# Optimization experiments

Hardware: AMD Instinct MI355X
Metric: run time of the kernel (lower is better)

## Reference

```python
import jax, jax.numpy as jnp
import numpy as np
from functools import partial

# dims matching init_kwargs
H = 512      # hidden_size
F = 2048     # ff_size
NH = 8       # num_heads
NL = 6       # num_layers
V = 1024     # vocab_size
T = 8        # sentence_length
S = 5        # n_sentences_in_paragraph
P = 16       # n_paragraphs_in_article
L = P * S * T          # article_length = 640
N = L + 1              # sequence length used by masks = 641
B = 16                 # batch
HD = H // NH           # head dim
LN_EPS = 1e-5
NEG = -1e9


def _build_mask():
    # pseudo_causal_masks[0] from the torch __init__: causal ~tril plus
    # blocking of within-paragraph sentence-0 key columns.
    a = np.ones((P, S, T, P, S, T), dtype=bool)
    j = np.arange(P)
    a[j, :, :, j, 0, :] = False
    a = a.reshape(L, L)
    causal = ~np.tril(np.ones((N, N), dtype=bool))
    m = causal.copy()
    m[:-1, 1:] = np.logical_and(a, causal[:-1, 1:])
    return m  # True = disallowed


def _build_pe():
    # sinusoidal pe exactly as in __init__ (div_term uses hidden_size in denom)
    pos = np.arange(N, dtype=np.float32)[:, None]
    div = np.exp(np.arange(0, H // 2, dtype=np.float32) * (-np.log(10000.0) / H))
    pe = np.zeros((N, H), dtype=np.float32)
    pe[:, 0::2] = np.sin(pos * div)
    pe[:, 1::2] = np.cos(pos * div)
    return pe


def setup_inputs() -> dict:
    key = jax.random.key(0)
    ks = jax.random.split(key, 12)
    sd = 0.02
    inp = {
        'tokens': jax.random.randint(ks[0], (B, N), 0, V),
        'attn_mask': jnp.asarray(_build_mask()),
        'pe': jnp.asarray(_build_pe()),
        'emb': jax.random.normal(ks[1], (V, H), jnp.float32) * sd,
        'qkv_w': jax.random.normal(ks[2], (NL, 3 * H, H), jnp.float32) * sd,
        'qkv_b': jnp.zeros((NL, 3 * H), jnp.float32),
        'out_w': jax.random.normal(ks[3], (NL, H, H), jnp.float32) * sd,
        'out_b': jnp.zeros((NL, H), jnp.float32),
        'ln1_g': jnp.ones((NL, H), jnp.float32),
        'ln1_b': jnp.zeros((NL, H), jnp.float32),
        'fc1_w': jax.random.normal(ks[4], (NL, F, H), jnp.float32) * sd,
        'fc1_b': jnp.zeros((NL, F), jnp.float32),
        'fc2_w': jax.random.normal(ks[5], (NL, H, F), jnp.float32) * sd,
        'fc2_b': jnp.zeros((NL, H), jnp.float32),
        'ln2_g': jnp.ones((NL, H), jnp.float32),
        'ln2_b': jnp.zeros((NL, H), jnp.float32),
        'lnf_g': jnp.ones((H,), jnp.float32),
        'lnf_b': jnp.zeros((H,), jnp.float32),
        'dep_w': jax.random.normal(ks[6], (V, H), jnp.float32) * sd,
        'dep_b': jnp.zeros((V,), jnp.float32),
    }
    return inp


def _ln(x, g, b):
    m = jnp.mean(x, axis=-1, keepdims=True)
    v = jnp.mean(jnp.square(x - m), axis=-1, keepdims=True)
    return (x - m) * jax.lax.rsqrt(v + LN_EPS) * g + b


def _encoder_layer(x, p, mask):
    qw, qb, ow, ob, g1, b1, w1, bb1, w2, bb2, g2, b2 = p
    Bsz, Nn, _ = x.shape
    qkv = x @ qw.T + qb                                   # [B,N,3H]
    q, k, v = jnp.split(qkv, 3, axis=-1)
    q = q.reshape(Bsz, Nn, NH, HD)
    k = k.reshape(Bsz, Nn, NH, HD)
    v = v.reshape(Bsz, Nn, NH, HD)
    scores = jnp.einsum('bqhd,bkhd->bhqk', q, k) / jnp.sqrt(jnp.asarray(HD, x.dtype))
    scores = jnp.where(mask[None, None], NEG, scores)
    att = jax.nn.softmax(scores, axis=-1)
    o = jnp.einsum('bhqk,bkhd->bqhd', att, v).reshape(Bsz, Nn, H)
    o = o @ ow.T + ob
    x = _ln(x + o, g1, b1)                                # post-LN (torch default)
    f = jax.nn.gelu(x @ w1.T + bb1, approximate=False) @ w2.T + bb2
    return _ln(x + f, g2, b2)


def reference(tokens, attn_mask, pe, emb, qkv_w, qkv_b, out_w, out_b,
              ln1_g, ln1_b, fc1_w, fc1_b, fc2_w, fc2_b, ln2_g, ln2_b,
              lnf_g, lnf_b, dep_w, dep_b):
    x = emb[tokens] + pe[None]                            # [B,N,H]
    layers = (qkv_w, qkv_b, out_w, out_b, ln1_g, ln1_b,
              fc1_w, fc1_b, fc2_w, fc2_b, ln2_g, ln2_b)

    def step(h, p):
        return _encoder_layer(h, p, attn_mask), None

    x, _ = jax.lax.scan(step, x, layers)
    x = _ln(x, lnf_g, lnf_b)
    return x @ dep_w.T + dep_b                            # [B,N,V] logits
```

## Files before the change

kernel.cpp:

```cpp
#include <hip/hip_runtime.h>
#include <stdint.h>

#define NSEQ 641
#define BATCH 16
#define MROWS (BATCH * NSEQ)
#define HID 512
#define FFD 2048
#define NHEAD 8
#define HDIM 64
#define NLAYER 6
#define VOCAB 1024
#define KPAD 704

typedef __bf16 bf16x8 __attribute__((ext_vector_type(8)));
typedef float  f32x4  __attribute__((ext_vector_type(4)));
typedef int    i32x4  __attribute__((ext_vector_type(4)));
typedef short  s16x8  __attribute__((ext_vector_type(8)));
typedef short  s16x4  __attribute__((ext_vector_type(4)));

#define EXP_C 0.18033688011112042f

__device__ __forceinline__ uint32_t swz(uint32_t b) { return b ^ (((b >> 7) & 7u) << 4); }
__device__ __forceinline__ uint32_t swz32(uint32_t b) { return b ^ (((b >> 7) & 3u) << 4); }

__device__ __forceinline__ int xcd_swz(int bid, int nwg) {
  int x = bid & 7, j = bid >> 3;
  int q = nwg >> 3, r = nwg & 7;
  return x * q + (x < r ? x : r) + j;
}

__device__ __forceinline__ unsigned short f2bf(float f) {
  uint32_t u = __builtin_bit_cast(uint32_t, f);
  u += 0x7FFFu + ((u >> 16) & 1u);
  return (unsigned short)(u >> 16);
}

__device__ __forceinline__ void gload16(const void* g, void* l) {
  __builtin_amdgcn_global_load_lds(
      (const __attribute__((address_space(1))) uint32_t*)g,
      (__attribute__((address_space(3))) uint32_t*)l, 16, 0, 0);
}

__device__ __forceinline__ bf16x8 ld_lds16(const void* p) {
  return __builtin_bit_cast(bf16x8, *(const i32x4*)p);
}

__global__ void cvt_kernel(const float* __restrict__ in,
                           unsigned short* __restrict__ out, int n) {
  int i = (blockIdx.x * 256 + threadIdx.x) * 4;
  if (i >= n) return;
  f32x4 v = *(const f32x4*)(in + i);
  s16x4 o;
  o[0] = (short)f2bf(v[0]); o[1] = (short)f2bf(v[1]);
  o[2] = (short)f2bf(v[2]); o[3] = (short)f2bf(v[3]);
  *(s16x4*)(out + i) = o;
}

__global__ void embed_kernel(const int* __restrict__ tok,
                             const float* __restrict__ emb,
                             const float* __restrict__ pe,
                             float* __restrict__ x,
                             unsigned short* __restrict__ xb) {
  int m = blockIdx.x;
  int n = m % NSEQ;
  int t = tok[m];
  int h = threadIdx.x * 4;
  f32x4 e = *(const f32x4*)(emb + (size_t)t * HID + h);
  f32x4 p = *(const f32x4*)(pe + (size_t)n * HID + h);
  f32x4 v = e + p;
  *(f32x4*)(x + (size_t)m * HID + h) = v;
  s16x4 o;
  o[0] = (short)f2bf(v[0]); o[1] = (short)f2bf(v[1]);
  o[2] = (short)f2bf(v[2]); o[3] = (short)f2bf(v[3]);
  *(s16x4*)(xb + (size_t)m * HID + h) = o;
}

__global__ __launch_bounds__(256) void ln_kernel(
    const float* __restrict__ in, const float* __restrict__ gg,
    const float* __restrict__ bb, float* __restrict__ xo,
    unsigned short* __restrict__ xbo, int rows) {
  int row = blockIdx.x * 4 + (threadIdx.x >> 6);
  if (row >= rows) return;
  int lane = threadIdx.x & 63;
  const float* p = in + (size_t)row * HID + lane * 8;
  f32x4 a0 = *(const f32x4*)p;
  f32x4 a1 = *(const f32x4*)(p + 4);
  float s = a0[0] + a0[1] + a0[2] + a0[3] + a1[0] + a1[1] + a1[2] + a1[3];
#pragma unroll
  for (int o = 32; o; o >>= 1) s += __shfl_xor(s, o);
  float mean = s * (1.0f / HID);
  float vs = 0.f;
#pragma unroll
  for (int j = 0; j < 4; ++j) { float d = a0[j] - mean; vs += d * d; }
#pragma unroll
  for (int j = 0; j < 4; ++j) { float d = a1[j] - mean; vs += d * d; }
#pragma unroll
  for (int o = 32; o; o >>= 1) vs += __shfl_xor(vs, o);
  float rstd = rsqrtf(vs * (1.0f / HID) + 1e-5f);
  f32x4 g0 = *(const f32x4*)(gg + lane * 8);
  f32x4 g1 = *(const f32x4*)(gg + lane * 8 + 4);
  f32x4 b0 = *(const f32x4*)(bb + lane * 8);
  f32x4 b1 = *(const f32x4*)(bb + lane * 8 + 4);
  f32x4 y0, y1;
  s16x8 ob;
#pragma unroll
  for (int j = 0; j < 4; ++j) {
    y0[j] = (a0[j] - mean) * rstd * g0[j] + b0[j];
    y1[j] = (a1[j] - mean) * rstd * g1[j] + b1[j];
    ob[j] = (short)f2bf(y0[j]);
    ob[j + 4] = (short)f2bf(y1[j]);
  }
  float* xp = xo + (size_t)row * HID + lane * 8;
  *(f32x4*)xp = y0;
  *(f32x4*)(xp + 4) = y1;
  *(s16x8*)(xbo + (size_t)row * HID + lane * 8) = ob;
}

__global__ __launch_bounds__(256) void vtrans_kernel(
    const unsigned short* __restrict__ V, unsigned short* __restrict__ vT) {
  const int kt = blockIdx.x;
  const int bh = blockIdx.y;
  const int k0 = kt * 64;
  const int tid = threadIdx.x;
  __shared__ unsigned short lds[64][68];
  const size_t src = (size_t)bh * (NSEQ * HDIM);
#pragma unroll
  for (int it = 0; it < 2; ++it) {
    int k = it * 32 + (tid >> 3);
    int d0 = (tid & 7) * 8;
    int kr = k0 + k;
    s16x8 v = {};
    if (kr < NSEQ) v = *(const s16x8*)(V + src + (size_t)kr * HDIM + d0);
    *(s16x8*)&lds[k][d0] = v;
  }
  __syncthreads();
  const int d = tid & 63;
  const int w = tid >> 6;
  const size_t dst = ((size_t)bh * 64 + d) * KPAD + k0;
#pragma unroll
  for (int it = 0; it < 2; ++it) {
    int kc = w + it * 4;
    s16x8 o;
#pragma unroll
    for (int i = 0; i < 8; ++i) o[i] = lds[kc * 8 + i][d];
    *(s16x8*)(vT + dst + kc * 8) = o;
  }
}

enum { EPI_QKV = 0, EPI_GELU = 1, EPI_RESID = 2, EPI_F32OUT = 3 };

template <int EPI, int BM>
__global__ __launch_bounds__(256, 3) void gemm_bt(
    const unsigned short* __restrict__ A, const unsigned short* __restrict__ W,
    const float* __restrict__ bias, const float* __restrict__ resid,
    void* __restrict__ out0, void* __restrict__ out1, void* __restrict__ out2,
    int M, int N, int K) {
  constexpr int ASZ = BM * 64;
  constexpr int BUF = ASZ + 8192;
  constexpr int MI = BM >> 5;
  constexpr int WROWS = BM >> 1;
  constexpr int ALOADS = ASZ / 4096;
  __shared__ char sm[3][BUF];
  const int tid = threadIdx.x, lane = tid & 63, wid = tid >> 6;
  const int wr = wid >> 1, wc = wid & 1;
  const int lg = lane >> 4, lc = lane & 15;

  const int nx = N >> 7;
  const int logical = xcd_swz(blockIdx.x, gridDim.x);
  const int m0 = (logical / nx) * BM, n0 = (logical % nx) * 128;

  f32x4 acc[MI][4] = {};

  auto stage = [&](int kt, char* dst) {
#pragma unroll
    for (int i = 0; i < ALOADS; ++i) {
      uint32_t P = (uint32_t)tid * 16 + i * 4096;
      uint32_t L = swz32(P);
      int row = (int)(L >> 6);
      uint32_t kb = L & 63u;
      int ma = m0 + row; if (ma >= M) ma = M - 1;
      gload16((const char*)A + ((size_t)ma * K + kt) * 2 + kb, dst + P);
    }
#pragma unroll
    for (int i = 0; i < 2; ++i) {
      uint32_t P = (uint32_t)tid * 16 + i * 4096;
      uint32_t L = swz32(P);
      int row = (int)(L >> 6);
      uint32_t kb = L & 63u;
      gload16((const char*)W + ((size_t)(n0 + row) * K + kt) * 2 + kb,
              dst + ASZ + P);
    }
  };

  const int nk = K >> 5;
  stage(0, sm[0]);
  stage(32, sm[1]);

  int bc = 0;
  for (int t = 0; t < nk; ++t) {
    if (t + 1 < nk) {
      if constexpr (ALOADS == 2) asm volatile("s_waitcnt vmcnt(4)" ::: "memory");
      else                       asm volatile("s_waitcnt vmcnt(3)" ::: "memory");
    } else {
      asm volatile("s_waitcnt vmcnt(0)" ::: "memory");
    }
    __builtin_amdgcn_sched_barrier(0);
    __builtin_amdgcn_s_barrier();
    __builtin_amdgcn_sched_barrier(0);
    if (t + 2 < nk) {
      int b2 = bc + 2; if (b2 >= 3) b2 -= 3;
      stage((t + 2) << 5, sm[b2]);
    }
    const char* buf = sm[bc];
    bf16x8 af[MI], bfr[4];
#pragma unroll
    for (int mi = 0; mi < MI; ++mi) {
      int row = wr * WROWS + mi * 16 + lc;
      af[mi] = ld_lds16(buf + swz32((uint32_t)row * 64 + (lg << 4)));
    }
#pragma unroll
    for (int ni = 0; ni < 4; ++ni) {
      int row = wc * 64 + ni * 16 + lc;
      bfr[ni] = ld_lds16(buf + ASZ + swz32((uint32_t)row * 64 + (lg << 4)));
    }
#pragma unroll
    for (int mi = 0; mi < MI; ++mi)
#pragma unroll
      for (int ni = 0; ni < 4; ++ni)
        acc[mi][ni] = __builtin_amdgcn_mfma_f32_16x16x32_bf16(af[mi], bfr[ni], acc[mi][ni], 0, 0, 0);
    asm volatile("s_waitcnt lgkmcnt(0)" ::: "memory");
    __builtin_amdgcn_sched_barrier(0);
    if (++bc == 3) bc = 0;
  }

#pragma unroll
  for (int mi = 0; mi < MI; ++mi) {
#pragma unroll
    for (int g = 0; g < 4; ++g) {
      int m = m0 + wr * WROWS + mi * 16 + lg * 4 + g;
      if (m >= M) continue;
      int bbq = 0, nn = 0;
      if (EPI == EPI_QKV) { bbq = m / NSEQ; nn = m - bbq * NSEQ; }
#pragma unroll
      for (int ni = 0; ni < 4; ++ni) {
        int c = n0 + wc * 64 + ni * 16 + lc;
        float v = acc[mi][ni][g] + bias[c];
        if (EPI == EPI_QKV) {
          int which = c >> 9, hh = (c >> 6) & 7, d = c & 63;
          unsigned short* dst = which == 0 ? (unsigned short*)out0
                              : which == 1 ? (unsigned short*)out1
                                           : (unsigned short*)out2;
          dst[(((size_t)bbq * NHEAD + hh) * NSEQ + nn) * HDIM + d] = f2bf(v);
        } else if (EPI == EPI_GELU) {
          v = 0.5f * v * (1.0f + erff(v * 0.70710678118654752f));
          ((unsigned short*)out0)[(size_t)m * N + c] = f2bf(v);
        } else if (EPI == EPI_RESID) {
          float* o = (float*)out0;
          o[(size_t)m * N + c] = v + resid[(size_t)m * N + c];
        } else {
          ((float*)out0)[(size_t)m * N + c] = v;
        }
      }
    }
  }
}

__global__ __launch_bounds__(256) void attn_kernel(
    const unsigned short* __restrict__ Q, const unsigned short* __restrict__ Kb,
    const unsigned short* __restrict__ vT, unsigned short* __restrict__ O) {
  const int logical = xcd_swz(blockIdx.x, gridDim.x);
  const int qt = logical % 11, bh = logical / 11;
  const int b = bh >> 3, h = bh & 7;
  const int q0 = qt * 64;
  const int tid = threadIdx.x, lane = tid & 63, w = tid >> 6;
  const int lg = lane >> 4, lc = lane & 15;
  __shared__ char sK[2][8192];
  __shared__ char sV[2][8192];
  __shared__ char sP[4][2048];

  const size_t base = (size_t)bh * (NSEQ * HDIM);
  const size_t baseT = (size_t)bh * (HDIM * KPAD);

  bf16x8 qf[2];
  {
    int qr = q0 + w * 16 + lc;
    if (qr > NSEQ - 1) qr = NSEQ - 1;
#pragma unroll
    for (int kk = 0; kk < 2; ++kk)
      qf[kk] = __builtin_bit_cast(
          bf16x8, *(const i32x4*)(Q + base + (size_t)qr * HDIM + kk * 32 + (lg << 3)));
  }

  f32x4 acc[4] = {};
  float lsum[4] = {0.f, 0.f, 0.f, 0.f};
  const int qrow_base = q0 + w * 16 + (lg << 2);

  int nkt = qt + 2;
  if (nkt > 11) nkt = 11;

  auto stage = [&](int kt, int bufi) {
    const int k0 = kt * 64;
#pragma unroll
    for (int i = 0; i < 2; ++i) {
      uint32_t P = w * 2048 + i * 1024 + lane * 16;
      uint32_t L = swz(P);
      int row = (int)(L >> 7);
      uint32_t kbyte = L & 127u;
      int kr = k0 + row; if (kr > NSEQ - 1) kr = NSEQ - 1;
      gload16((const char*)(Kb + base + (size_t)kr * HDIM) + kbyte,
              sK[bufi] + w * 2048 + i * 1024);
      gload16((const char*)(vT + baseT + (size_t)row * KPAD + k0) + kbyte,
              sV[bufi] + w * 2048 + i * 1024);
    }
  };

  stage(0, 0);
  __syncthreads();

  for (int kt = 0; kt < nkt; ++kt) {
    if (kt + 1 < nkt) stage(kt + 1, (kt + 1) & 1);
    const char* bK = sK[kt & 1];
    const char* bV = sV[kt & 1];
    const int k0 = kt * 64;

    f32x4 s[4] = {};
#pragma unroll
    for (int nt = 0; nt < 4; ++nt) {
#pragma unroll
      for (int kk = 0; kk < 2; ++kk) {
        int row = nt * 16 + lc;
        bf16x8 kf = ld_lds16(bK + swz((uint32_t)row * 128 + kk * 64 + (lg << 4)));
        s[nt] = __builtin_amdgcn_mfma_f32_16x16x32_bf16(qf[kk], kf, s[nt], 0, 0, 0);
      }
    }

    if (kt < qt) {
#pragma unroll
      for (int g = 0; g < 4; ++g)
#pragma unroll
        for (int nt = 0; nt < 4; ++nt) {
          float p = exp2f(s[nt][g] * EXP_C);
          s[nt][g] = p;
          lsum[g] += p;
        }
    } else if (kt == qt) {
#pragma unroll
      for (int g = 0; g < 4; ++g) {
        int q = qrow_base + g;
        int pp = q / 40;
        int lo = pp * 40 + 1, hi = pp * 40 + 8;
#pragma unroll
        for (int nt = 0; nt < 4; ++nt) {
          int k = k0 + nt * 16 + lc;
          bool ok = ((k <= q) || (k >= lo && k <= hi)) && (k < NSEQ);
          float p = ok ? exp2f(s[nt][g] * EXP_C) : 0.f;
          s[nt][g] = p;
          lsum[g] += p;
        }
      }
    } else {
#pragma unroll
      for (int g = 0; g < 4; ++g) {
        int q = qrow_base + g;
        int pp = q / 40;
        int lo = pp * 40 + 1, hi = pp * 40 + 8;
#pragma unroll
        for (int nt = 0; nt < 4; ++nt) {
          int k = k0 + nt * 16 + lc;
          bool ok = (k >= lo && k <= hi) && (k < NSEQ);
          float p = ok ? exp2f(s[nt][g] * EXP_C) : 0.f;
          s[nt][g] = p;
          lsum[g] += p;
        }
      }
    }

#pragma unroll
    for (int g = 0; g < 4; ++g) {
      int row = (lg << 2) + g;
#pragma unroll
      for (int nt = 0; nt < 4; ++nt) {
        int col = nt * 16 + lc;
        *(short*)(sP[w] + swz((uint32_t)row * 128 + col * 2)) = (short)f2bf(s[nt][g]);
      }
    }
#pragma unroll
    for (int kk = 0; kk < 2; ++kk) {
      bf16x8 pa = ld_lds16(sP[w] + swz((uint32_t)lc * 128 + kk * 64 + (lg << 4)));
#pragma unroll
      for (int nt = 0; nt < 4; ++nt) {
        int rowv = nt * 16 + lc;
        bf16x8 vf = ld_lds16(bV + swz((uint32_t)rowv * 128 + kk * 64 + (lg << 4)));
        acc[nt] = __builtin_amdgcn_mfma_f32_16x16x32_bf16(pa, vf, acc[nt], 0, 0, 0);
      }
    }
    __syncthreads();
  }

#pragma unroll
  for (int o = 1; o < 16; o <<= 1)
#pragma unroll
    for (int g = 0; g < 4; ++g) lsum[g] += __shfl_xor(lsum[g], o);

#pragma unroll
  for (int g = 0; g < 4; ++g) {
    int q = qrow_base + g;
    if (q >= NSEQ) continue;
    float inv = 1.0f / lsum[g];
#pragma unroll
    for (int nt = 0; nt < 4; ++nt) {
      int d = nt * 16 + lc;
      O[((size_t)b * NSEQ + q) * HID + h * HDIM + d] = f2bf(acc[nt][g] * inv);
    }
  }
}

extern "C" void kernel_launch(void* const* d_in, const int* in_sizes, int n_in,
                              void* d_out, int out_size, void* d_ws, size_t ws_size,
                              hipStream_t stream) {
  const int*   tok   = (const int*)d_in[0];
  const float* pe    = (const float*)d_in[2];
  const float* emb   = (const float*)d_in[3];
  const float* qkv_w = (const float*)d_in[4];
  const float* qkv_b = (const float*)d_in[5];
  const float* out_w = (const float*)d_in[6];
  const float* out_b = (const float*)d_in[7];
  const float* ln1_g = (const float*)d_in[8];
  const float* ln1_b = (const float*)d_in[9];
  const float* fc1_w = (const float*)d_in[10];
  const float* fc1_b = (const float*)d_in[11];
  const float* fc2_w = (const float*)d_in[12];
  const float* fc2_b = (const float*)d_in[13];
  const float* ln2_g = (const float*)d_in[14];
  const float* ln2_b = (const float*)d_in[15];
  const float* lnf_g = (const float*)d_in[16];
  const float* lnf_b = (const float*)d_in[17];
  const float* dep_w = (const float*)d_in[18];
  const float* dep_b = (const float*)d_in[19];

  const size_t SZ_QKV = (size_t)1536 * 512;
  const size_t SZ_OUT = (size_t)512 * 512;
  const size_t SZ_FC1 = (size_t)2048 * 512;
  const size_t SZ_FC2 = (size_t)512 * 2048;
  const size_t SZ_DEP = (size_t)VOCAB * 512;

  char* w = (char*)d_ws;
  float* x = (float*)w;            w += (size_t)MROWS * HID * 4;
  unsigned short* xb = (unsigned short*)w; w += (size_t)MROWS * HID * 2;
  unsigned short* qb = (unsigned short*)w; w += (size_t)BATCH * NHEAD * NSEQ * HDIM * 2;
  unsigned short* kb = (unsigned short*)w; w += (size_t)BATCH * NHEAD * NSEQ * HDIM * 2;
  unsigned short* vb = (unsigned short*)w; w += (size_t)BATCH * NHEAD * NSEQ * HDIM * 2;
  unsigned short* ao = (unsigned short*)w; w += (size_t)BATCH * NHEAD * NSEQ * HDIM * 2;
  unsigned short* mid = qb;
  unsigned short* vT = (unsigned short*)w; w += (size_t)BATCH * NHEAD * HDIM * KPAD * 2;

  size_t used = (size_t)(w - (char*)d_ws);
  size_t all_w_bytes = (NLAYER * (SZ_QKV + SZ_OUT + SZ_FC1 + SZ_FC2) + SZ_DEP) * 2;
  bool upfront = ws_size >= used + all_w_bytes;

  unsigned short *wq_all, *wo_all, *w1_all, *w2_all, *wd;
  if (upfront) {
    wq_all = (unsigned short*)w; w += NLAYER * SZ_QKV * 2;
    wo_all = (unsigned short*)w; w += NLAYER * SZ_OUT * 2;
    w1_all = (unsigned short*)w; w += NLAYER * SZ_FC1 * 2;
    w2_all = (unsigned short*)w; w += NLAYER * SZ_FC2 * 2;
    wd     = (unsigned short*)w; w += SZ_DEP * 2;
    cvt_kernel<<<dim3((NLAYER * SZ_QKV) / 1024), 256, 0, stream>>>(qkv_w, wq_all, NLAYER * SZ_QKV);
    cvt_kernel<<<dim3((NLAYER * SZ_OUT) / 1024), 256, 0, stream>>>(out_w, wo_all, NLAYER * SZ_OUT);
    cvt_kernel<<<dim3((NLAYER * SZ_FC1) / 1024), 256, 0, stream>>>(fc1_w, w1_all, NLAYER * SZ_FC1);
    cvt_kernel<<<dim3((NLAYER * SZ_FC2) / 1024), 256, 0, stream>>>(fc2_w, w2_all, NLAYER * SZ_FC2);
    cvt_kernel<<<dim3(SZ_DEP / 1024), 256, 0, stream>>>(dep_w, wd, SZ_DEP);
  } else {
    wq_all = (unsigned short*)w; w += SZ_QKV * 2;
    wo_all = (unsigned short*)w; w += SZ_OUT * 2;
    w1_all = (unsigned short*)w; w += SZ_FC1 * 2;
    w2_all = (unsigned short*)w; w += SZ_FC2 * 2;
    wd     = (unsigned short*)w; w += SZ_DEP * 2;
    cvt_kernel<<<dim3(SZ_DEP / 1024), 256, 0, stream>>>(dep_w, wd, SZ_DEP);
  }

  embed_kernel<<<dim3(MROWS), 128, 0, stream>>>(tok, emb, pe, x, xb);

  const int lnBlocks = (MROWS + 3) / 4;
  for (int l = 0; l < NLAYER; ++l) {
    unsigned short *wq, *wo, *w1, *w2;
    if (upfront) {
      wq = wq_all + l * SZ_QKV; wo = wo_all + l * SZ_OUT;
      w1 = w1_all + l * SZ_FC1; w2 = w2_all + l * SZ_FC2;
    } else {
      wq = wq_all; wo = wo_all; w1 = w1_all; w2 = w2_all;
      cvt_kernel<<<dim3(SZ_QKV / 1024), 256, 0, stream>>>(qkv_w + l * SZ_QKV, wq, SZ_QKV);
      cvt_kernel<<<dim3(SZ_OUT / 1024), 256, 0, stream>>>(out_w + l * SZ_OUT, wo, SZ_OUT);
      cvt_kernel<<<dim3(SZ_FC1 / 1024), 256, 0, stream>>>(fc1_w + l * SZ_FC1, w1, SZ_FC1);
      cvt_kernel<<<dim3(SZ_FC2 / 1024), 256, 0, stream>>>(fc2_w + l * SZ_FC2, w2, SZ_FC2);
    }

    gemm_bt<EPI_QKV, 128><<<dim3(12 * 81), 256, 0, stream>>>(
        xb, wq, qkv_b + l * 1536, nullptr, qb, kb, vb, MROWS, 1536, 512);
    vtrans_kernel<<<dim3(11, 128), 256, 0, stream>>>(vb, vT);
    attn_kernel<<<dim3(11 * 128), 256, 0, stream>>>(qb, kb, vT, ao);
    gemm_bt<EPI_RESID, 64><<<dim3(4 * 161), 256, 0, stream>>>(
        ao, wo, out_b + l * 512, x, x, nullptr, nullptr, MROWS, 512, 512);
    ln_kernel<<<dim3(lnBlocks), 256, 0, stream>>>(x, ln1_g + l * 512, ln1_b + l * 512, x, xb, MROWS);
    gemm_bt<EPI_GELU, 128><<<dim3(16 * 81), 256, 0, stream>>>(
        xb, w1, fc1_b + l * 2048, nullptr, mid, nullptr, nullptr, MROWS, 2048, 512);
    gemm_bt<EPI_RESID, 64><<<dim3(4 * 161), 256, 0, stream>>>(
        mid, w2, fc2_b + l * 512, x, x, nullptr, nullptr, MROWS, 512, 2048);
    ln_kernel<<<dim3(lnBlocks), 256, 0, stream>>>(x, ln2_g + l * 512, ln2_b + l * 512, x, xb, MROWS);
  }

  ln_kernel<<<dim3(lnBlocks), 256, 0, stream>>>(x, lnf_g, lnf_b, x, xb, MROWS);
  gemm_bt<EPI_F32OUT, 64><<<dim3(8 * 161), 256, 0, stream>>>(
      xb, wd, dep_b, nullptr, d_out, nullptr, nullptr, MROWS, VOCAB, 512);
}
```

Measured before the change: 1.395 ms.

## Keep residual stream in bf16 and add attention occupancy bound

Drops the fp32 residual buffer, so the embedding, the residual GEMM epilogues and the layernorms read and write the hidden state only as bf16, with a separate bf16 sum buffer feeding each layernorm. This roughly halves the memory traffic of the residual and LN passes. The attention kernel's LDS is merged into one array and it gets a launch bound of 4 blocks per SM. The cost is accuracy, since the residual stream is rounded to bf16 every layer.

```diff
diff --git a/kernel.cpp b/kernel.cpp
--- a/kernel.cpp
+++ b/kernel.cpp
@@ -35,6 +35,11 @@
   return (unsigned short)(u >> 16);
 }
 
+__device__ __forceinline__ float bf2f(unsigned short u) {
+  uint32_t t = ((uint32_t)u) << 16;
+  return __builtin_bit_cast(float, t);
+}
+
 __device__ __forceinline__ void gload16(const void* g, void* l) {
   __builtin_amdgcn_global_load_lds(
       (const __attribute__((address_space(1))) uint32_t*)g,
@@ -59,7 +64,6 @@
 __global__ void embed_kernel(const int* __restrict__ tok,
                              const float* __restrict__ emb,
                              const float* __restrict__ pe,
-                             float* __restrict__ x,
                              unsigned short* __restrict__ xb) {
   int m = blockIdx.x;
   int n = m % NSEQ;
@@ -68,7 +72,6 @@
   f32x4 e = *(const f32x4*)(emb + (size_t)t * HID + h);
   f32x4 p = *(const f32x4*)(pe + (size_t)n * HID + h);
   f32x4 v = e + p;
-  *(f32x4*)(x + (size_t)m * HID + h) = v;
   s16x4 o;
   o[0] = (short)f2bf(v[0]); o[1] = (short)f2bf(v[1]);
   o[2] = (short)f2bf(v[2]); o[3] = (short)f2bf(v[3]);
@@ -76,24 +79,22 @@
 }
 
 __global__ __launch_bounds__(256) void ln_kernel(
-    const float* __restrict__ in, const float* __restrict__ gg,
-    const float* __restrict__ bb, float* __restrict__ xo,
-    unsigned short* __restrict__ xbo, int rows) {
+    const unsigned short* __restrict__ in, const float* __restrict__ gg,
+    const float* __restrict__ bb, unsigned short* __restrict__ out, int rows) {
   int row = blockIdx.x * 4 + (threadIdx.x >> 6);
   if (row >= rows) return;
   int lane = threadIdx.x & 63;
-  const float* p = in + (size_t)row * HID + lane * 8;
-  f32x4 a0 = *(const f32x4*)p;
-  f32x4 a1 = *(const f32x4*)(p + 4);
-  float s = a0[0] + a0[1] + a0[2] + a0[3] + a1[0] + a1[1] + a1[2] + a1[3];
+  s16x8 raw = *(const s16x8*)(in + (size_t)row * HID + lane * 8);
+  float a[8];
+#pragma unroll
+  for (int j = 0; j < 8; ++j) a[j] = bf2f((unsigned short)raw[j]);
+  float s = a[0] + a[1] + a[2] + a[3] + a[4] + a[5] + a[6] + a[7];
 #pragma unroll
   for (int o = 32; o; o >>= 1) s += __shfl_xor(s, o);
   float mean = s * (1.0f / HID);
   float vs = 0.f;
 #pragma unroll
-  for (int j = 0; j < 4; ++j) { float d = a0[j] - mean; vs += d * d; }
-#pragma unroll
-  for (int j = 0; j < 4; ++j) { float d = a1[j] - mean; vs += d * d; }
+  for (int j = 0; j < 8; ++j) { float d = a[j] - mean; vs += d * d; }
 #pragma unroll
   for (int o = 32; o; o >>= 1) vs += __shfl_xor(vs, o);
   float rstd = rsqrtf(vs * (1.0f / HID) + 1e-5f);
@@ -101,19 +102,13 @@
   f32x4 g1 = *(const f32x4*)(gg + lane * 8 + 4);
   f32x4 b0 = *(const f32x4*)(bb + lane * 8);
   f32x4 b1 = *(const f32x4*)(bb + lane * 8 + 4);
-  f32x4 y0, y1;
   s16x8 ob;
 #pragma unroll
   for (int j = 0; j < 4; ++j) {
-    y0[j] = (a0[j] - mean) * rstd * g0[j] + b0[j];
-    y1[j] = (a1[j] - mean) * rstd * g1[j] + b1[j];
-    ob[j] = (short)f2bf(y0[j]);
-    ob[j + 4] = (short)f2bf(y1[j]);
-  }
-  float* xp = xo + (size_t)row * HID + lane * 8;
-  *(f32x4*)xp = y0;
-  *(f32x4*)(xp + 4) = y1;
-  *(s16x8*)(xbo + (size_t)row * HID + lane * 8) = ob;
+    ob[j]     = (short)f2bf((a[j]     - mean) * rstd * g0[j] + b0[j]);
+    ob[j + 4] = (short)f2bf((a[j + 4] - mean) * rstd * g1[j] + b1[j]);
+  }
+  *(s16x8*)(out + (size_t)row * HID + lane * 8) = ob;
 }
 
 __global__ __launch_bounds__(256) void vtrans_kernel(
@@ -152,7 +147,7 @@
 template <int EPI, int BM>
 __global__ __launch_bounds__(256, 3) void gemm_bt(
     const unsigned short* __restrict__ A, const unsigned short* __restrict__ W,
-    const float* __restrict__ bias, const float* __restrict__ resid,
+    const float* __restrict__ bias, const unsigned short* __restrict__ resid,
     void* __restrict__ out0, void* __restrict__ out1, void* __restrict__ out2,
     int M, int N, int K) {
   constexpr int ASZ = BM * 64;
@@ -255,8 +250,8 @@
           v = 0.5f * v * (1.0f + erff(v * 0.70710678118654752f));
           ((unsigned short*)out0)[(size_t)m * N + c] = f2bf(v);
         } else if (EPI == EPI_RESID) {
-          float* o = (float*)out0;
-          o[(size_t)m * N + c] = v + resid[(size_t)m * N + c];
+          ((unsigned short*)out0)[(size_t)m * N + c] =
+              f2bf(v + bf2f(resid[(size_t)m * N + c]));
         } else {
           ((float*)out0)[(size_t)m * N + c] = v;
         }
@@ -265,7 +260,7 @@
   }
 }
 
-__global__ __launch_bounds__(256) void attn_kernel(
+__global__ __launch_bounds__(256, 4) void attn_kernel(
     const unsigned short* __restrict__ Q, const unsigned short* __restrict__ Kb,
     const unsigned short* __restrict__ vT, unsigned short* __restrict__ O) {
   const int logical = xcd_swz(blockIdx.x, gridDim.x);
@@ -274,9 +269,7 @@
   const int q0 = qt * 64;
   const int tid = threadIdx.x, lane = tid & 63, w = tid >> 6;
   const int lg = lane >> 4, lc = lane & 15;
-  __shared__ char sK[2][8192];
-  __shared__ char sV[2][8192];
-  __shared__ char sP[4][2048];
+  __shared__ char smem[40960];
 
   const size_t base = (size_t)bh * (NSEQ * HDIM);
   const size_t baseT = (size_t)bh * (HDIM * KPAD);
@@ -308,9 +301,9 @@
       uint32_t kbyte = L & 127u;
       int kr = k0 + row; if (kr > NSEQ - 1) kr = NSEQ - 1;
       gload16((const char*)(Kb + base + (size_t)kr * HDIM) + kbyte,
-              sK[bufi] + w * 2048 + i * 1024);
+              smem + bufi * 8192 + w * 2048 + i * 1024);
       gload16((const char*)(vT + baseT + (size_t)row * KPAD + k0) + kbyte,
-              sV[bufi] + w * 2048 + i * 1024);
+              smem + 16384 + bufi * 8192 + w * 2048 + i * 1024);
     }
   };
 
@@ -319,8 +312,9 @@
 
   for (int kt = 0; kt < nkt; ++kt) {
     if (kt + 1 < nkt) stage(kt + 1, (kt + 1) & 1);
-    const char* bK = sK[kt & 1];
-    const char* bV = sV[kt & 1];
+    const char* bK = smem + (kt & 1) * 8192;
+    const char* bV = smem + 16384 + (kt & 1) * 8192;
+    char* sPw = smem + 32768 + w * 2048;
     const int k0 = kt * 64;
 
     f32x4 s[4] = {};
@@ -381,12 +375,12 @@
 #pragma unroll
       for (int nt = 0; nt < 4; ++nt) {
         int col = nt * 16 + lc;
-        *(short*)(sP[w] + swz((uint32_t)row * 128 + col * 2)) = (short)f2bf(s[nt][g]);
+        *(short*)(sPw + swz((uint32_t)row * 128 + col * 2)) = (short)f2bf(s[nt][g]);
       }
     }
 #pragma unroll
     for (int kk = 0; kk < 2; ++kk) {
-      bf16x8 pa = ld_lds16(sP[w] + swz((uint32_t)lc * 128 + kk * 64 + (lg << 4)));
+      bf16x8 pa = ld_lds16(sPw + swz((uint32_t)lc * 128 + kk * 64 + (lg << 4)));
 #pragma unroll
       for (int nt = 0; nt < 4; ++nt) {
         int rowv = nt * 16 + lc;
@@ -445,8 +439,8 @@
   const size_t SZ_DEP = (size_t)VOCAB * 512;
 
   char* w = (char*)d_ws;
-  float* x = (float*)w;            w += (size_t)MROWS * HID * 4;
   unsigned short* xb = (unsigned short*)w; w += (size_t)MROWS * HID * 2;
+  unsigned short* sb = (unsigned short*)w; w += (size_t)MROWS * HID * 2;
   unsigned short* qb = (unsigned short*)w; w += (size_t)BATCH * NHEAD * NSEQ * HDIM * 2;
   unsigned short* kb = (unsigned short*)w; w += (size_t)BATCH * NHEAD * NSEQ * HDIM * 2;
   unsigned short* vb = (unsigned short*)w; w += (size_t)BATCH * NHEAD * NSEQ * HDIM * 2;
@@ -479,7 +473,7 @@
     cvt_kernel<<<dim3(SZ_DEP / 1024), 256, 0, stream>>>(dep_w, wd, SZ_DEP);
   }
 
-  embed_kernel<<<dim3(MROWS), 128, 0, stream>>>(tok, emb, pe, x, xb);
+  embed_kernel<<<dim3(MROWS), 128, 0, stream>>>(tok, emb, pe, xb);
 
   const int lnBlocks = (MROWS + 3) / 4;
   for (int l = 0; l < NLAYER; ++l) {
@@ -500,16 +494,16 @@
     vtrans_kernel<<<dim3(11, 128), 256, 0, stream>>>(vb, vT);
     attn_kernel<<<dim3(11 * 128), 256, 0, stream>>>(qb, kb, vT, ao);
     gemm_bt<EPI_RESID, 64><<<dim3(4 * 161), 256, 0, stream>>>(
-        ao, wo, out_b + l * 512, x, x, nullptr, nullptr, MROWS, 512, 512);
-    ln_kernel<<<dim3(lnBlocks), 256, 0, stream>>>(x, ln1_g + l * 512, ln1_b + l * 512, x, xb, MROWS);
+        ao, wo, out_b + l * 512, xb, sb, nullptr, nullptr, MROWS, 512, 512);
+    ln_kernel<<<dim3(lnBlocks), 256, 0, stream>>>(sb, ln1_g + l * 512, ln1_b + l * 512, xb, MROWS);
     gemm_bt<EPI_GELU, 128><<<dim3(16 * 81), 256, 0, stream>>>(
         xb, w1, fc1_b + l * 2048, nullptr, mid, nullptr, nullptr, MROWS, 2048, 512);
     gemm_bt<EPI_RESID, 64><<<dim3(4 * 161), 256, 0, stream>>>(
-        mid, w2, fc2_b + l * 512, x, x, nullptr, nullptr, MROWS, 512, 2048);
-    ln_kernel<<<dim3(lnBlocks), 256, 0, stream>>>(x, ln2_g + l * 512, ln2_b + l * 512, x, xb, MROWS);
-  }
-
-  ln_kernel<<<dim3(lnBlocks), 256, 0, stream>>>(x, lnf_g, lnf_b, x, xb, MROWS);
+        mid, w2, fc2_b + l * 512, xb, sb, nullptr, nullptr, MROWS, 512, 2048);
+    ln_kernel<<<dim3(lnBlocks), 256, 0, stream>>>(sb, ln2_g + l * 512, ln2_b + l * 512, xb, MROWS);
+  }
+
+  ln_kernel<<<dim3(lnBlocks), 256, 0, stream>>>(xb, lnf_g, lnf_b, xb, MROWS);
   gemm_bt<EPI_F32OUT, 64><<<dim3(8 * 161), 256, 0, stream>>>(
       xb, wd, dep_b, nullptr, d_out, nullptr, nullptr, MROWS, VOCAB, 512);
 }
```

Measured after the change: 1.326 ms. 1.05x faster.
